# Optimization experiments

Measured on AMD Instinct MI355X. Metric: run time of the kernel, lower is better.

Reference implementation:

```python
import jax, jax.numpy as jnp
import numpy as np

N_NODES = 100000
N_EDGES = 3200000
IN_DIM = 128
HID = 64


def _gcn_conv(x, src, dst, norm, W, b, n_nodes):
    # x: [N, Fin]; PyG GCNConv: h = x @ W^T, propagate with sym norm, + bias
    h = x @ W.T                                  # [N, Fout]
    msg = h[src] * norm[:, None]                 # gather + scale, [E', Fout]
    out = jax.ops.segment_sum(msg, dst, num_segments=n_nodes)  # scatter-add
    return out + b


def _build_norm(edge_index, n_nodes):
    # add self-loops, compute D^-1/2 A D^-1/2 edge weights
    loops = jnp.arange(n_nodes, dtype=edge_index.dtype)
    src = jnp.concatenate([edge_index[0], loops])
    dst = jnp.concatenate([edge_index[1], loops])
    deg = jax.ops.segment_sum(jnp.ones_like(dst, dtype=jnp.float32), dst,
                              num_segments=n_nodes)
    dinv = jnp.where(deg > 0, jax.lax.rsqrt(jnp.maximum(deg, 1.0)), 0.0)
    norm = dinv[src] * dinv[dst]
    return src, dst, norm


def setup_inputs() -> dict:
    key = jax.random.key(0)
    k = jax.random.split(key, 8)
    x = jax.random.normal(k[0], (N_NODES, IN_DIM), dtype=jnp.float32)
    edge_index = jax.random.randint(k[1], (2, N_EDGES), 0, N_NODES, dtype=jnp.int64)
    s1 = 1.0 / np.sqrt(IN_DIM)
    s2 = 1.0 / np.sqrt(HID)
    W1 = jax.random.uniform(k[2], (HID, IN_DIM), jnp.float32, -s1, s1)
    b1 = jnp.zeros((HID,), jnp.float32)
    W2 = jax.random.uniform(k[3], (HID, HID), jnp.float32, -s2, s2)
    b2 = jnp.zeros((HID,), jnp.float32)
    Wc = jax.random.uniform(k[4], (1, HID), jnp.float32, -s2, s2)
    bc = jax.random.uniform(k[5], (1,), jnp.float32, -s2, s2)
    return {"x": x, "edge_index": edge_index, "W1": W1, "b1": b1,
            "W2": W2, "b2": b2, "Wc": Wc, "bc": bc}


def reference(x, edge_index, W1, b1, W2, b2, Wc, bc):
    n = x.shape[0]
    src, dst, norm = _build_norm(edge_index, n)
    h = _gcn_conv(x, src, dst, norm, W1, b1, n)
    h = jax.nn.relu(h)
    h = _gcn_conv(h, src, dst, norm, W2, b2, n)
    return h @ Wc.T + bc                          # [N, 1]
```

## Files before the change

### kernel.cpp

```cpp
#include <hip/hip_runtime.h>
#include <hip/hip_bf16.h>
#include <hip/hip_fp16.h>

#define N_NODES 100000
#define N_EDGES 3200000
#define F_IN    128
#define F_H     64

#define NBUCK 256
#define NPB   391
#define SRC_BITS 17

#define BH_T 256
#define BH_C 16384
__global__ __launch_bounds__(BH_T) void k_bhist(const int* __restrict__ dst,
                                                int* __restrict__ bcount) {
    __shared__ int lc[NBUCK];
    int t = threadIdx.x;
    lc[t] = 0;
    __syncthreads();
    long long e0 = (long long)blockIdx.x * BH_C;
    long long e1 = e0 + BH_C; if (e1 > N_EDGES) e1 = N_EDGES;
    for (long long e = e0 + t; e < e1; e += BH_T)
        atomicAdd(&lc[dst[e] / NPB], 1);
    __syncthreads();
    int c = lc[t];
    if (c) atomicAdd(&bcount[t], c);
}

__global__ __launch_bounds__(NBUCK) void k_bscan(const int* __restrict__ bcount,
                                                 int* __restrict__ bbase,
                                                 int* __restrict__ bcur,
                                                 int* __restrict__ row_ptr) {
    __shared__ int s[NBUCK];
    int t = threadIdx.x;
    int c = bcount[t];
    s[t] = c;
    __syncthreads();
    for (int off = 1; off < NBUCK; off <<= 1) {
        int v = (t >= off) ? s[t - off] : 0;
        __syncthreads();
        s[t] += v;
        __syncthreads();
    }
    int ex = s[t] - c;
    bbase[t] = ex;
    bcur[t]  = ex;
    if (t == NBUCK - 1) {
        bbase[NBUCK] = s[t];
        row_ptr[N_NODES] = s[t];
    }
}

__global__ __launch_bounds__(64) void k_wc2(const float* __restrict__ W2,
                                            const float* __restrict__ Wc,
                                            const float* __restrict__ b2,
                                            const float* __restrict__ bc,
                                            float* __restrict__ wc2,
                                            float* __restrict__ c0) {
    int k = threadIdx.x;
    float s = 0.0f;
#pragma unroll 8
    for (int f = 0; f < F_H; f++) s += Wc[f] * W2[f * F_H + k];
    wc2[k] = s;
    float p = Wc[k] * b2[k];
#pragma unroll
    for (int off = 32; off > 0; off >>= 1) p += __shfl_xor(p, off, 64);
    if (k == 0) c0[0] = p + bc[0];
}

#define PA_T   256
#define PA_C   4096
#define PA_PER (PA_C / PA_T)
__global__ __launch_bounds__(PA_T) void k_partA(const int* __restrict__ src,
                                                const int* __restrict__ dst,
                                                int* __restrict__ bucket_cursor,
                                                int* __restrict__ packT) {
    __shared__ int lcount[NBUCK];
    __shared__ int lstart[NBUCK];
    __shared__ int loffs[NBUCK];
    __shared__ int lbase[NBUCK];
    __shared__ int s_pack[PA_C];
    __shared__ unsigned char s_bkt[PA_C];
    __shared__ int ltot;
    int t = threadIdx.x;
    long long e0 = (long long)blockIdx.x * PA_C;
    if (t < NBUCK) lcount[t] = 0;
    __syncthreads();
    int ep[PA_PER];
    short eb[PA_PER];
#pragma unroll
    for (int i = 0; i < PA_PER; i++) {
        long long e = e0 + i * PA_T + t;
        if (e < N_EDGES) {
            int es = src[e], ed = dst[e];
            int b = ed / NPB;
            eb[i] = (short)b;
            ep[i] = ((ed - b * NPB) << SRC_BITS) | es;
            atomicAdd(&lcount[b], 1);
        } else eb[i] = -1;
    }
    __syncthreads();
    if (t < 64) {
        int base = t * 4;
        int c0 = lcount[base], c1 = lcount[base + 1], c2 = lcount[base + 2], c3 = lcount[base + 3];
        int ssum = c0 + c1 + c2 + c3;
        int sc = ssum;
#pragma unroll
        for (int off = 1; off < 64; off <<= 1) {
            int v = __shfl_up(sc, off, 64);
            if (t >= off) sc += v;
        }
        int ex = sc - ssum;
        lstart[base]     = ex;
        lstart[base + 1] = ex + c0;
        lstart[base + 2] = ex + c0 + c1;
        lstart[base + 3] = ex + c0 + c1 + c2;
        if (t == 63) ltot = sc;
    }
    __syncthreads();
    if (t < NBUCK) {
        loffs[t] = lstart[t];
        int c = lcount[t];
        lbase[t] = c ? atomicAdd(&bucket_cursor[t], c) : 0;
    }
    __syncthreads();
#pragma unroll
    for (int i = 0; i < PA_PER; i++) {
        if (eb[i] >= 0) {
            int idx = atomicAdd(&loffs[eb[i]], 1);
            s_pack[idx] = ep[i];
            s_bkt[idx] = (unsigned char)eb[i];
        }
    }
    __syncthreads();
    int tot = ltot;
    for (int i = t; i < tot; i += PA_T) {
        int b = s_bkt[i];
        int addr = lbase[b] + (i - lstart[b]);
        packT[addr] = s_pack[i];
    }
}

#define PB_T   1024
#define PB_CAP 16384
__global__ __launch_bounds__(PB_T) void k_partB(const int* __restrict__ bbase,
                                                const int* __restrict__ packT,
                                                int* __restrict__ row_ptr,
                                                float* __restrict__ dinv,
                                                int* __restrict__ srcs) {
    __shared__ int lhist[NPB];
    __shared__ int lcur[NPB];
    __shared__ int s_out[PB_CAP];
    int b = blockIdx.x;
    int node0 = b * NPB;
    int node1 = min(node0 + NPB, N_NODES);
    int nloc = node1 - node0;
    int beg = bbase[b];
    int end = bbase[b + 1];
    int len = end - beg;
    int t = threadIdx.x;
    const int SMASK = (1 << SRC_BITS) - 1;

    for (int i = t; i < NPB; i += PB_T) lhist[i] = 0;
    __syncthreads();
    for (int i = t; i < len; i += PB_T)
        atomicAdd(&lhist[packT[beg + i] >> SRC_BITS], 1);
    __syncthreads();
    if (t < 64) {
        int base = t * 7;
        int c[7]; int ssum = 0;
#pragma unroll
        for (int j = 0; j < 7; j++) {
            int idx = base + j;
            c[j] = (idx < NPB) ? lhist[idx] : 0;
            ssum += c[j];
        }
        int sc = ssum;
#pragma unroll
        for (int off = 1; off < 64; off <<= 1) {
            int v = __shfl_up(sc, off, 64);
            if (t >= off) sc += v;
        }
        int ex = sc - ssum;
#pragma unroll
        for (int j = 0; j < 7; j++) {
            int idx = base + j;
            if (idx < NPB) lcur[idx] = ex;
            ex += c[j];
        }
    }
    __syncthreads();
    for (int i = t; i < nloc; i += PB_T) {
        row_ptr[node0 + i] = beg + lcur[i];
        dinv[node0 + i] = rsqrtf((float)(lhist[i] + 1));
    }
    __syncthreads();
    if (len <= PB_CAP) {
        for (int i = t; i < len; i += PB_T) {
            int pk = packT[beg + i];
            int idx = atomicAdd(&lcur[pk >> SRC_BITS], 1);
            s_out[idx] = pk & SMASK;
        }
        __syncthreads();
        for (int i = t; i < len; i += PB_T)
            srcs[beg + i] = s_out[i];
    } else {
        for (int i = t; i < len; i += PB_T) {
            int pk = packT[beg + i];
            int idx = atomicAdd(&lcur[pk >> SRC_BITS], 1);
            srcs[beg + idx] = pk & SMASK;
        }
    }
}

#define GT   256
#define NTB  128
#define KT   64
#define WTS  68

__global__ __launch_bounds__(GT) void k_gemm1(const float* __restrict__ x,
                                              const float* __restrict__ W1,
                                              const float* __restrict__ dinv,
                                              __half* __restrict__ hs) {
    __shared__ float wT[KT * WTS];
    __shared__ float xT[KT * NTB];
    int t = threadIdx.x;
    int node0 = blockIdx.x * NTB;
    int lane = t & 63, wv = t >> 6;
    int fi = lane & 15, ni = lane >> 4;
    int n0 = wv * 32 + ni * 8;

    float acc[4][8];
#pragma unroll
    for (int r = 0; r < 4; r++)
#pragma unroll
        for (int c = 0; c < 8; c++) acc[r][c] = 0.0f;

    for (int p = 0; p < 2; p++) {
        int k0 = p * KT;
        if (p) __syncthreads();
        {
            int f = t & 63, kq = t >> 6;
            const float4* wp = (const float4*)&W1[(size_t)f * F_IN + k0 + kq * 16];
#pragma unroll
            for (int j = 0; j < 4; j++) {
                float4 v = wp[j];
                int kl = kq * 16 + 4 * j;
                wT[(kl + 0) * WTS + f] = v.x;
                wT[(kl + 1) * WTS + f] = v.y;
                wT[(kl + 2) * WTS + f] = v.z;
                wT[(kl + 3) * WTS + f] = v.w;
            }
        }
        {
            int n = t & 127, half = t >> 7;
            int node = node0 + n;
#pragma unroll
            for (int j = 0; j < 8; j++) {
                int ku = half * 8 + j;
                float4 v = make_float4(0.f, 0.f, 0.f, 0.f);
                if (node < N_NODES)
                    v = *(const float4*)&x[(size_t)node * F_IN + k0 + 4 * ku];
                int kl = 4 * ku;
                xT[(kl + 0) * NTB + n] = v.x;
                xT[(kl + 1) * NTB + n] = v.y;
                xT[(kl + 2) * NTB + n] = v.z;
                xT[(kl + 3) * NTB + n] = v.w;
            }
        }
        __syncthreads();
#pragma unroll 8
        for (int k = 0; k < KT; k++) {
            float4 wf = *(const float4*)&wT[k * WTS + fi * 4];
            float4 xa = *(const float4*)&xT[k * NTB + n0];
            float4 xb = *(const float4*)&xT[k * NTB + n0 + 4];
            float wr[4] = {wf.x, wf.y, wf.z, wf.w};
            float xv[8] = {xa.x, xa.y, xa.z, xa.w, xb.x, xb.y, xb.z, xb.w};
#pragma unroll
            for (int r = 0; r < 4; r++)
#pragma unroll
                for (int c = 0; c < 8; c++) acc[r][c] += wr[r] * xv[c];
        }
    }
#pragma unroll
    for (int c = 0; c < 8; c++) {
        int node = node0 + n0 + c;
        if (node < N_NODES) {
            float dv = dinv[node];
            __half2 h0 = __floats2half2_rn(acc[0][c] * dv, acc[1][c] * dv);
            __half2 h1 = __floats2half2_rn(acc[2][c] * dv, acc[3][c] * dv);
            __half2* p = (__half2*)&hs[(size_t)node * F_H + fi * 4];
            p[0] = h0; p[1] = h1;
        }
    }
}

__global__ void k_agg1q(const int* __restrict__ row_ptr, const int* __restrict__ srcs,
                        const __half* __restrict__ hs, const float* __restrict__ dinv,
                        const float* __restrict__ b1, const float* __restrict__ wc2,
                        float* __restrict__ q) {
    unsigned tid = blockIdx.x * blockDim.x + threadIdx.x;
    unsigned node = tid >> 6;
    int lane = tid & 63;
    if (node >= N_NODES) return;
    int up = lane >> 5;
    int fp = lane & 31;
    const __half2* hs2 = (const __half2*)hs;

    int beg = row_ptr[node], end = row_ptr[node + 1];
    float2 acc = make_float2(0.0f, 0.0f);
    if (up == 0) {
        float2 s = __half22float2(hs2[(size_t)node * 32 + fp]);
        acc.x = s.x; acc.y = s.y;
    }
    int j = beg;
    for (; j + 16 <= end; j += 16) {
        int s[16];
#pragma unroll
        for (int u = 0; u < 16; u++) s[u] = srcs[j + u];
#pragma unroll
        for (int u = 0; u < 8; u++) {
            int sel = up ? s[2 * u + 1] : s[2 * u];
            float2 v = __half22float2(hs2[(size_t)sel * 32 + fp]);
            acc.x += v.x; acc.y += v.y;
        }
    }
    for (; j + 2 <= end; j += 2) {
        int sel = up ? srcs[j + 1] : srcs[j];
        float2 v = __half22float2(hs2[(size_t)sel * 32 + fp]);
        acc.x += v.x; acc.y += v.y;
    }
    if (j < end && up == 0) {
        float2 v = __half22float2(hs2[(size_t)srcs[j] * 32 + fp]);
        acc.x += v.x; acc.y += v.y;
    }
    acc.x += __shfl_xor(acc.x, 32, 64);
    acc.y += __shfl_xor(acc.y, 32, 64);
    float dv = dinv[node];
    float2 bb = *(const float2*)&b1[2 * fp];
    float2 ww = *(const float2*)&wc2[2 * fp];
    float z0 = fmaxf(dv * acc.x + bb.x, 0.0f);
    float z1 = fmaxf(dv * acc.y + bb.y, 0.0f);
    float p = z0 * ww.x + z1 * ww.y;
#pragma unroll
    for (int off = 16; off > 0; off >>= 1)
        p += __shfl_xor(p, off, 64);
    if (lane == 0) q[node] = dv * p;
}

__global__ void k_final(const int* __restrict__ row_ptr, const int* __restrict__ srcs,
                        const float* __restrict__ q, const float* __restrict__ dinv,
                        const float* __restrict__ c0, float* __restrict__ out) {
    int node = blockIdx.x * blockDim.x + threadIdx.x;
    if (node >= N_NODES) return;
    int beg = row_ptr[node], end = row_ptr[node + 1];
    float acc = q[node];
    int j = beg;
    for (; j + 4 <= end; j += 4) {
        int s0 = srcs[j], s1 = srcs[j + 1], s2 = srcs[j + 2], s3 = srcs[j + 3];
        float a0 = q[s0], a1 = q[s1], a2 = q[s2], a3 = q[s3];
        acc += (a0 + a1) + (a2 + a3);
    }
    for (; j < end; j++) acc += q[srcs[j]];
    out[node] = dinv[node] * acc + c0[0];
}

extern "C" void kernel_launch(void* const* d_in, const int* in_sizes, int n_in,
                              void* d_out, int out_size, void* d_ws, size_t ws_size,
                              hipStream_t stream) {
    const float* x  = (const float*)d_in[0];
    const int*   ei = (const int*)d_in[1];
    const int*   src = ei;
    const int*   dst = ei + N_EDGES;
    const float* W1 = (const float*)d_in[2];
    const float* b1 = (const float*)d_in[3];
    const float* W2 = (const float*)d_in[4];
    const float* b2 = (const float*)d_in[5];
    const float* Wc = (const float*)d_in[6];
    const float* bc = (const float*)d_in[7];
    float* out = (float*)d_out;

    char* w = (char*)d_ws;
    int*    bcount  = (int*)w;    w += NBUCK * 4;
    int*    bbase   = (int*)w;    w += (NBUCK + 1) * 4;
    int*    bcur    = (int*)w;    w += NBUCK * 4;
    float*  wc2     = (float*)w;  w += 64 * 4;
    float*  c0      = (float*)w;  w += 4 * 4;
    int*    row_ptr = (int*)w;    w += ((size_t)N_NODES + 4) * 4;
    float*  dinv    = (float*)w;  w += (size_t)N_NODES * 4;
    float*  q       = (float*)w;  w += (size_t)N_NODES * 4;
    int*    srcs    = (int*)w;    w += (size_t)N_EDGES * 4;
    __half* bufA    = (__half*)w; w += (size_t)N_NODES * F_H * 2;
    int*    packT   = (int*)w;    w += (size_t)N_EDGES * 4;

    const int TB = 256;
    const int NB_BH = (int)(((long long)N_EDGES + BH_C - 1) / BH_C);
    const int NB_PA = (int)(((long long)N_EDGES + PA_C - 1) / PA_C);
    const int NB_G  = (N_NODES + NTB - 1) / NTB;

    hipMemsetAsync(bcount, 0, NBUCK * 4, stream);
    k_bhist<<<NB_BH, BH_T, 0, stream>>>(dst, bcount);
    k_bscan<<<1, NBUCK, 0, stream>>>(bcount, bbase, bcur, row_ptr);
    k_wc2  <<<1, 64, 0, stream>>>(W2, Wc, b2, bc, wc2, c0);
    k_partA<<<NB_PA, PA_T, 0, stream>>>(src, dst, bcur, packT);
    k_partB<<<NBUCK, PB_T, 0, stream>>>(bbase, packT, row_ptr, dinv, srcs);

    k_gemm1<<<NB_G, GT, 0, stream>>>(x, W1, dinv, bufA);
    k_agg1q<<<((unsigned)N_NODES * 64 + TB - 1) / TB, TB, 0, stream>>>(row_ptr, srcs, bufA, dinv, b1, wc2, q);

    k_final<<<(N_NODES + TB - 1) / TB, TB, 0, stream>>>(row_ptr, srcs, q, dinv, c0, out);
}
```

Measured before the change: 317.2 us.

## Split layer-1 aggregation into four feature-slice passes with planar half2 layout

The GEMM output is stored as four planar slices of 16 features each, with a zero sentinel row for padding. Aggregation then runs in four passes, each gathering only a 3.2 MB slice, so each pass's working set fits in cache. Each wave handles 8 edges at once with 8 lanes per edge, and source indices are loaded coalesced and broadcast via shuffles. The partition kernel also doubles its block and chunk size. The cost is four launches, four re-reads of srcs and row_ptr, and a read-modify-write accumulation of q across passes.

```diff
diff --git a/kernel.cpp b/kernel.cpp
--- a/kernel.cpp
+++ b/kernel.cpp
@@ -69,8 +69,8 @@
     if (k == 0) c0[0] = p + bc[0];
 }
 
-#define PA_T   256
-#define PA_C   4096
+#define PA_T   512
+#define PA_C   8192
 #define PA_PER (PA_C / PA_T)
 __global__ __launch_bounds__(PA_T) void k_partA(const int* __restrict__ src,
                                                 const int* __restrict__ dst,
@@ -218,11 +218,12 @@
 #define NTB  128
 #define KT   64
 #define WTS  68
+#define QSTRIDE ((size_t)(N_NODES + 1) * 8)
 
 __global__ __launch_bounds__(GT) void k_gemm1(const float* __restrict__ x,
                                               const float* __restrict__ W1,
                                               const float* __restrict__ dinv,
-                                              __half* __restrict__ hs) {
+                                              __half2* __restrict__ hq) {
     __shared__ float wT[KT * WTS];
     __shared__ float xT[KT * NTB];
     int t = threadIdx.x;
@@ -286,67 +287,69 @@
 #pragma unroll
     for (int c = 0; c < 8; c++) {
         int node = node0 + n0 + c;
-        if (node < N_NODES) {
-            float dv = dinv[node];
+        if (node <= N_NODES) {
+            float dv = (node < N_NODES) ? dinv[node] : 0.0f;
             __half2 h0 = __floats2half2_rn(acc[0][c] * dv, acc[1][c] * dv);
             __half2 h1 = __floats2half2_rn(acc[2][c] * dv, acc[3][c] * dv);
-            __half2* p = (__half2*)&hs[(size_t)node * F_H + fi * 4];
+            __half2* p = hq + (size_t)(fi >> 2) * QSTRIDE + (size_t)node * 8 + 2 * (fi & 3);
             p[0] = h0; p[1] = h1;
         }
     }
 }
 
-__global__ void k_agg1q(const int* __restrict__ row_ptr, const int* __restrict__ srcs,
-                        const __half* __restrict__ hs, const float* __restrict__ dinv,
-                        const float* __restrict__ b1, const float* __restrict__ wc2,
-                        float* __restrict__ q) {
+__global__ void k_aggq(const int* __restrict__ row_ptr, const int* __restrict__ srcs,
+                       const __half2* __restrict__ hq, const float* __restrict__ dinv,
+                       const float* __restrict__ b1, const float* __restrict__ wc2,
+                       float* __restrict__ q, int pass) {
     unsigned tid = blockIdx.x * blockDim.x + threadIdx.x;
     unsigned node = tid >> 6;
     int lane = tid & 63;
     if (node >= N_NODES) return;
-    int up = lane >> 5;
-    int fp = lane & 31;
-    const __half2* hs2 = (const __half2*)hs;
+    int d = lane & 7, r = lane >> 3;
+    const __half2* hp = hq + (size_t)pass * QSTRIDE;
 
     int beg = row_ptr[node], end = row_ptr[node + 1];
     float2 acc = make_float2(0.0f, 0.0f);
-    if (up == 0) {
-        float2 s = __half22float2(hs2[(size_t)node * 32 + fp]);
+    if (r == 0) {
+        float2 s = __half22float2(hp[(size_t)node * 8 + d]);
         acc.x = s.x; acc.y = s.y;
     }
     int j = beg;
-    for (; j + 16 <= end; j += 16) {
-        int s[16];
-#pragma unroll
-        for (int u = 0; u < 16; u++) s[u] = srcs[j + u];
+    for (; j + 64 <= end; j += 64) {
+        int sv = srcs[j + lane];
 #pragma unroll
         for (int u = 0; u < 8; u++) {
-            int sel = up ? s[2 * u + 1] : s[2 * u];
-            float2 v = __half22float2(hs2[(size_t)sel * 32 + fp]);
+            int sel = __shfl(sv, u * 8 + r, 64);
+            float2 v = __half22float2(hp[(size_t)sel * 8 + d]);
             acc.x += v.x; acc.y += v.y;
         }
     }
-    for (; j + 2 <= end; j += 2) {
-        int sel = up ? srcs[j + 1] : srcs[j];
-        float2 v = __half22float2(hs2[(size_t)sel * 32 + fp]);
+    for (; j + 8 <= end; j += 8) {
+        int sel = srcs[j + r];
+        float2 v = __half22float2(hp[(size_t)sel * 8 + d]);
         acc.x += v.x; acc.y += v.y;
     }
-    if (j < end && up == 0) {
-        float2 v = __half22float2(hs2[(size_t)srcs[j] * 32 + fp]);
+    if (j < end) {
+        int sel = (j + r < end) ? srcs[j + r] : N_NODES;
+        float2 v = __half22float2(hp[(size_t)sel * 8 + d]);
         acc.x += v.x; acc.y += v.y;
     }
-    acc.x += __shfl_xor(acc.x, 32, 64);
-    acc.y += __shfl_xor(acc.y, 32, 64);
+    acc.x += __shfl_xor(acc.x, 8, 64);  acc.y += __shfl_xor(acc.y, 8, 64);
+    acc.x += __shfl_xor(acc.x, 16, 64); acc.y += __shfl_xor(acc.y, 16, 64);
+    acc.x += __shfl_xor(acc.x, 32, 64); acc.y += __shfl_xor(acc.y, 32, 64);
     float dv = dinv[node];
-    float2 bb = *(const float2*)&b1[2 * fp];
-    float2 ww = *(const float2*)&wc2[2 * fp];
-    float z0 = fmaxf(dv * acc.x + bb.x, 0.0f);
-    float z1 = fmaxf(dv * acc.y + bb.y, 0.0f);
-    float p = z0 * ww.x + z1 * ww.y;
-#pragma unroll
-    for (int off = 16; off > 0; off >>= 1)
-        p += __shfl_xor(p, off, 64);
-    if (lane == 0) q[node] = dv * p;
+    int f0 = pass * 16 + 2 * d;
+    float z0 = fmaxf(dv * acc.x + b1[f0], 0.0f);
+    float z1 = fmaxf(dv * acc.y + b1[f0 + 1], 0.0f);
+    float p = z0 * wc2[f0] + z1 * wc2[f0 + 1];
+    p += __shfl_xor(p, 1, 64);
+    p += __shfl_xor(p, 2, 64);
+    p += __shfl_xor(p, 4, 64);
+    if (lane == 0) {
+        if (pass == 0)      q[node] = p;
+        else if (pass < 3)  q[node] += p;
+        else                q[node] = dv * (q[node] + p);
+    }
 }
 
 __global__ void k_final(const int* __restrict__ row_ptr, const int* __restrict__ srcs,
@@ -382,17 +385,17 @@
     float* out = (float*)d_out;
 
     char* w = (char*)d_ws;
-    int*    bcount  = (int*)w;    w += NBUCK * 4;
-    int*    bbase   = (int*)w;    w += (NBUCK + 1) * 4;
-    int*    bcur    = (int*)w;    w += NBUCK * 4;
-    float*  wc2     = (float*)w;  w += 64 * 4;
-    float*  c0      = (float*)w;  w += 4 * 4;
-    int*    row_ptr = (int*)w;    w += ((size_t)N_NODES + 4) * 4;
-    float*  dinv    = (float*)w;  w += (size_t)N_NODES * 4;
-    float*  q       = (float*)w;  w += (size_t)N_NODES * 4;
-    int*    srcs    = (int*)w;    w += (size_t)N_EDGES * 4;
-    __half* bufA    = (__half*)w; w += (size_t)N_NODES * F_H * 2;
-    int*    packT   = (int*)w;    w += (size_t)N_EDGES * 4;
+    int*     bcount  = (int*)w;     w += NBUCK * 4;
+    int*     bbase   = (int*)w;     w += (NBUCK + 1) * 4;
+    int*     bcur    = (int*)w;     w += NBUCK * 4;
+    float*   wc2     = (float*)w;   w += 64 * 4;
+    float*   c0      = (float*)w;   w += 4 * 4;
+    int*     row_ptr = (int*)w;     w += ((size_t)N_NODES + 4) * 4;
+    float*   dinv    = (float*)w;   w += (size_t)N_NODES * 4;
+    float*   q       = (float*)w;   w += (size_t)N_NODES * 4;
+    int*     srcs    = (int*)w;     w += (size_t)N_EDGES * 4;
+    __half2* hq      = (__half2*)w; w += 4 * QSTRIDE * 4;
+    int*     packT   = (int*)w;     w += (size_t)N_EDGES * 4;
 
     const int TB = 256;
     const int NB_BH = (int)(((long long)N_EDGES + BH_C - 1) / BH_C);
@@ -406,8 +409,11 @@
     k_partA<<<NB_PA, PA_T, 0, stream>>>(src, dst, bcur, packT);
     k_partB<<<NBUCK, PB_T, 0, stream>>>(bbase, packT, row_ptr, dinv, srcs);
 
-    k_gemm1<<<NB_G, GT, 0, stream>>>(x, W1, dinv, bufA);
-    k_agg1q<<<((unsigned)N_NODES * 64 + TB - 1) / TB, TB, 0, stream>>>(row_ptr, srcs, bufA, dinv, b1, wc2, q);
+    k_gemm1<<<NB_G, GT, 0, stream>>>(x, W1, dinv, hq);
+
+    const int NB_AG = (int)(((unsigned)N_NODES * 64 + TB - 1) / TB);
+    for (int p = 0; p < 4; p++)
+        k_aggq<<<NB_AG, TB, 0, stream>>>(row_ptr, srcs, hq, dinv, b1, wc2, q, p);
 
     k_final<<<(N_NODES + TB - 1) / TB, TB, 0, stream>>>(row_ptr, srcs, q, dinv, c0, out);
 }
```

After: 425.3 us. 34.1% more time.
